# Kernel tuning notes

Measured on AMD Instinct MI355X. Metric: run time of the kernel, lower is better.

Reference implementation:

```python
import jax, jax.numpy as jnp
import numpy as np

R = 2
TAU = 0.1
EPS = 1e-7

# normalized 3x3 Sobel kernels (kornia SpatialGradient, normalized=True -> /8)
_GX = jnp.array([[-1., 0., 1.], [-2., 0., 2.], [-1., 0., 1.]], dtype=jnp.float32) / 8.0
_GY = _GX.T

K = 2 * R - 1  # 3
_HORIZ = jnp.zeros((K, K), jnp.float32).at[R - 1, :].set(1.0)
_VERT = jnp.zeros((K, K), jnp.float32).at[:, R - 1].set(1.0)
_LEAD = jnp.eye(K, dtype=jnp.float32)
_CNT = jnp.fliplr(jnp.eye(K, dtype=jnp.float32))


def _conv2d_same(x, k2d, mode):
    # depthwise 'same' cross-correlation, x: (B,C,H,W), k2d: (k,k)
    C = x.shape[1]
    p = k2d.shape[-1] // 2
    xp = jnp.pad(x, ((0, 0), (0, 0), (p, p), (p, p)), mode=mode)
    kern = jnp.broadcast_to(k2d[None, None], (C, 1) + k2d.shape)
    return jax.lax.conv_general_dilated(
        xp, kern, (1, 1), 'VALID',
        dimension_numbers=('NCHW', 'OIHW', 'NCHW'),
        feature_group_count=C)


def _grad_angles(t):
    # kornia SpatialGradient pads with replicate ('edge')
    gx = _conv2d_same(t, _GX, 'edge')
    gy = _conv2d_same(t, _GY, 'edge')
    grad_xx = _conv2d_same(gx, _GX, 'edge')
    grad_xy = _conv2d_same(gy, _GX, 'edge')
    grad_yy = _conv2d_same(gy, _GY, 'edge')
    theta = jnp.arctan(grad_yy * jnp.sign(-grad_xy + EPS) / (grad_xx + EPS))
    angle = theta * (180.0 / np.pi)
    return jnp.where(angle < 0, angle + 180.0, angle)


def _nms_loss(true_labels, pred_labels):
    angle = _grad_angles(true_labels)
    mask = (true_labels > 0).astype(jnp.float32)

    th_h = mask * (((angle >= 0) & (angle < 22.5)) | ((angle >= 157.5) & (angle < 180))).astype(jnp.float32)
    th_cd = mask * ((angle >= 22.5) & (angle < 67.5)).astype(jnp.float32)
    th_v = mask * ((angle >= 67.5) & (angle < 112.5)).astype(jnp.float32)
    th_ld = mask * ((angle > 112.5) & (angle < 157.5)).astype(jnp.float32)

    e = jnp.exp(pred_labels * TAU)

    def term(th, kern):
        f = _conv2d_same(e, kern, 'reflect')  # kornia filter2D default border 'reflect'
        return th * jnp.log(jnp.clip(e / (f + EPS), EPS, 1.0))

    total = (term(th_h, _HORIZ) + term(th_v, _VERT) +
             term(th_ld, _LEAD) + term(th_cd, _CNT))
    # sum over (C,H,W) per sample, mean over batch, negate
    return -jnp.mean(jnp.sum(total, axis=(1, 2, 3)))


def setup_inputs() -> dict:
    key = jax.random.key(0)
    k1, k2 = jax.random.split(key)
    B, C, H, W = 4, 19, 512, 512
    true_labels = jax.random.normal(k1, (B, C, H, W), dtype=jnp.float32)
    pred_labels = jax.random.normal(k2, (B, C, H, W), dtype=jnp.float32)
    return {"true_labels": true_labels, "pred_labels": pred_labels}


def reference(true_labels, pred_labels):
    return _nms_loss(true_labels, pred_labels)
```

## Files before the change

### kernel.cpp

```cpp
#include <hip/hip_runtime.h>

#define BAND 16
#define NITER (BAND + 4)
#define NSLOT 1024

__global__ __launch_bounds__(256) void nms_loss_kernel(
    const float* __restrict__ tl, const float* __restrict__ pl,
    double* __restrict__ acc_d, float* __restrict__ acc_f,
    int H, int W)
{
    const int y0  = blockIdx.x * BAND;
    const int ch  = blockIdx.y;
    const float* tc = tl + (size_t)ch * H * W;
    const float* pc = pl + (size_t)ch * H * W;
    const int tid  = threadIdx.x;
    const int lane = tid & 63;
    const int c0 = tid << 1;
    const int oa = min(max(c0 - 2, 0), W - 2);
    const int oc = min(c0 + 2, W - 2);
    const bool eL = (c0 == 0), eR = (c0 == W - 2);
    const float eL2 = eL ? 2.f : 0.f, eR2 = eR ? 2.f : 0.f;

    float P1h[5][2], P2h[5][2], P3h[5][2];
    float eh[3][4], tch[3][2];
    float t6[6], p6[6];

    #define LOADROW(I) {                                                            \
        int tr_ = y0 - 2 + (I); tr_ = min(max(tr_, 0), H - 1);                       \
        int pr_ = y0 - 3 + (I); pr_ = pr_ < 0 ? -pr_ : (pr_ >= H ? 2*H-2-pr_ : pr_); \
        const float* tb_ = tc + (size_t)tr_ * W;                                     \
        const float* pb_ = pc + (size_t)pr_ * W;                                     \
        float2 a_ = *(const float2*)(tb_ + oa), b_ = *(const float2*)(tb_ + c0),     \
               c_ = *(const float2*)(tb_ + oc);                                      \
        t6[0]=a_.x; t6[1]=a_.y; t6[2]=b_.x; t6[3]=b_.y; t6[4]=c_.x; t6[5]=c_.y;      \
        a_ = *(const float2*)(pb_ + oa); b_ = *(const float2*)(pb_ + c0);            \
        c_ = *(const float2*)(pb_ + oc);                                             \
        p6[0]=a_.x; p6[1]=a_.y; p6[2]=b_.x; p6[3]=b_.y; p6[4]=c_.x; p6[5]=c_.y;      \
        float g0_ = t6[0];                                                           \
        t6[0] = eL ? t6[1] : t6[0];                                                  \
        t6[1] = eL ? g0_   : t6[1];                                                  \
        float g4_ = t6[4];                                                           \
        t6[4] = eR ? t6[5] : t6[4];                                                  \
        t6[5] = eR ? g4_   : t6[5]; }

    #define CONSUME(K) {                                                             \
        eh[0][0]=eh[1][0]; eh[0][1]=eh[1][1]; eh[0][2]=eh[1][2]; eh[0][3]=eh[1][3];  \
        eh[1][0]=eh[2][0]; eh[1][1]=eh[2][1]; eh[1][2]=eh[2][2]; eh[1][3]=eh[2][3];  \
        tch[0][0]=tch[1][0]; tch[0][1]=tch[1][1];                                    \
        tch[1][0]=tch[2][0]; tch[1][1]=tch[2][1];                                    \
        float s04 = t6[0] + t6[4], s13 = t6[1] + t6[3];                              \
        P1h[K][0] = fmaf(-2.f, t6[2], s04);                                          \
        P3h[K][0] = fmaf(6.f, t6[2], fmaf(4.f, s13, s04));                           \
        P2h[K][0] = fmaf(2.f, t6[3] - t6[1], t6[4] - t6[0]);                         \
        float s04b = t6[1] + t6[5], s13b = t6[2] + t6[4];                            \
        P1h[K][1] = fmaf(-2.f, t6[3], s04b);                                         \
        P3h[K][1] = fmaf(6.f, t6[3], fmaf(4.f, s13b, s04b));                         \
        P2h[K][1] = fmaf(2.f, t6[4] - t6[2], t6[5] - t6[1]);                         \
        P1h[K][0] = fmaf(eL2, t6[2] - t6[3], P1h[K][0]);                             \
        P1h[K][1] = fmaf(eR2, t6[3] - t6[2], P1h[K][1]);                             \
        tch[2][0] = t6[2]; tch[2][1] = t6[3];                                        \
        eh[2][0] = __expf(0.1f * p6[1]);                                             \
        eh[2][1] = __expf(0.1f * p6[2]);                                             \
        eh[2][2] = __expf(0.1f * p6[3]);                                             \
        eh[2][3] = __expf(0.1f * p6[4]); }

    #define OUTPUT(I, K) if ((I) >= 4) {                                             \
        const int y = y0 + (I) - 4;                                                  \
        const int s0=((K)+1)%5, s1=((K)+2)%5, s2=((K)+3)%5, s3=((K)+4)%5, s4=(K);    \
        const bool ytop = (y == 0), ybot = (y == H - 1);                             \
        _Pragma("unroll")                                                            \
        for (int j = 0; j < 2; ++j) {                                                \
            float a04 = P1h[s0][j] + P1h[s4][j], a13 = P1h[s1][j] + P1h[s3][j];      \
            float xx = fmaf(6.f, P1h[s2][j], fmaf(4.f, a13, a04));                   \
            float xy = fmaf(2.f, P2h[s3][j] - P2h[s1][j], P2h[s4][j] - P2h[s0][j]);  \
            float yy = fmaf(-2.f, P3h[s2][j], P3h[s0][j] + P3h[s4][j]);              \
            if (ytop) {                                                              \
                xx += P1h[s3][j] - P1h[s2][j];                                       \
                xy += P2h[s3][j] - P2h[s2][j];                                       \
                yy += P3h[s2][j] - P3h[s3][j];                                       \
            } else if (ybot) {                                                       \
                xx += P1h[s1][j] - P1h[s2][j];                                       \
                xy += P2h[s2][j] - P2h[s1][j];                                       \
                yy += P3h[s2][j] - P3h[s1][j];                                       \
            }                                                                        \
            if (tch[0][j] > 0.f) {                                                   \
                float den = xx + 6.4e-6f;                                            \
                float sa  = 6.4e-6f - xy;                                            \
                float ax = fabsf(den), ay = fabsf(yy);                               \
                bool isH = ay < 0.41421356f * ax;                                    \
                bool isV = ay >= 2.41421356f * ax;                                   \
                bool qp  = ((yy * sa) * den) > 0.f;                                  \
                float ec = eh[1][j + 1];                                             \
                float n1 = isH ? eh[1][j + 2] : (isV ? eh[2][j + 1]                  \
                                : (qp ? eh[2][j] : eh[2][j + 2]));                   \
                float n2 = isH ? eh[1][j]     : (isV ? eh[0][j + 1]                  \
                                : (qp ? eh[0][j + 2] : eh[0][j]));                   \
                partial += __logf(__fdividef(ec, ec + n1 + n2 + 1e-7f));             \
            }                                                                        \
        } }

    LOADROW(0)

    float partial = 0.f;

    #pragma unroll 1
    for (int mm = 0; mm < 4; ++mm) {
        #pragma unroll
        for (int k = 0; k < 5; ++k) {
            const int i = mm * 5 + k;
            CONSUME(k)
            if (i + 1 < NITER) LOADROW(i + 1)
            OUTPUT(i, k)
        }
    }

    for (int off = 32; off > 0; off >>= 1)
        partial += __shfl_down(partial, off, 64);
    if (lane == 0) {
        int fid = (blockIdx.y * gridDim.x + blockIdx.x) * 4 + (tid >> 6);
        if (acc_d) atomicAdd(&acc_d[fid & (NSLOT - 1)], (double)partial);
        else       atomicAdd(acc_f, partial);
    }
}

__global__ void finalize_kernel(const double* acc_d, float* out,
                                int use_double, float inv_b)
{
    if (use_double) {
        int l = threadIdx.x;
        double s = 0.0;
        for (int i = l; i < NSLOT; i += 64) s += acc_d[i];
        for (int off = 32; off > 0; off >>= 1) s += __shfl_down(s, off, 64);
        if (l == 0) out[0] = (float)(-s * (double)inv_b);
    } else {
        if (threadIdx.x == 0) out[0] = -out[0] * inv_b;
    }
}

extern "C" void kernel_launch(void* const* d_in, const int* in_sizes, int n_in,
                              void* d_out, int out_size, void* d_ws, size_t ws_size,
                              hipStream_t stream)
{
    const float* tl = (const float*)d_in[0];
    const float* pl = (const float*)d_in[1];
    float* out = (float*)d_out;

    const int H = 512, W = 512, B = 4;

    double* acc_d = nullptr;
    float* acc_f = nullptr;
    int use_double = 0;
    if (ws_size >= NSLOT * sizeof(double)) {
        acc_d = (double*)d_ws;
        use_double = 1;
        hipMemsetAsync(acc_d, 0, NSLOT * sizeof(double), stream);
    } else {
        acc_f = out;
        hipMemsetAsync(out, 0, sizeof(float), stream);
    }

    dim3 grid(H / BAND, 76, 1);
    nms_loss_kernel<<<grid, 256, 0, stream>>>(tl, pl, acc_d, acc_f, H, W);
    finalize_kernel<<<1, 64, 0, stream>>>(acc_d, out, use_double, 1.0f / (float)B);
}
```

Measured before the change: 61.33 us.

## Use packed float2 math, fully unroll rows, and halve band height

Horizontal and vertical Sobel partial sums move to two-wide float vectors so the compiler can emit packed FP32 FMA/add instructions. The row loop is fully unrolled with modular register indexing, which removes the eh/tch shift copies. The band height drops from 16 to 8, doubling the number of blocks for more parallelism. The cost is more redundant halo row loads and exp work per output row, since each band rereads four extra rows.

After: 55.01 us, median of 2. 10.3% less time.

```diff
diff --git a/kernel.cpp b/kernel.cpp
--- a/kernel.cpp
+++ b/kernel.cpp
@@ -1,8 +1,15 @@
 #include <hip/hip_runtime.h>
 
-#define BAND 16
+#define BAND 8
 #define NITER (BAND + 4)
 #define NSLOT 1024
+
+typedef float v2f __attribute__((ext_vector_type(2)));
+
+__device__ __forceinline__ v2f fma2k(float k, v2f a, v2f b) {
+    v2f vk = {k, k};
+    return __builtin_elementwise_fma(vk, a, b);
+}
 
 __global__ __launch_bounds__(256) void nms_loss_kernel(
     const float* __restrict__ tl, const float* __restrict__ pl,
@@ -21,8 +28,9 @@
     const bool eL = (c0 == 0), eR = (c0 == W - 2);
     const float eL2 = eL ? 2.f : 0.f, eR2 = eR ? 2.f : 0.f;
 
-    float P1h[5][2], P2h[5][2], P3h[5][2];
-    float eh[3][4], tch[3][2];
+    v2f P1v[5], P2v[5], P3v[5];
+    float eh[3][4];
+    v2f tch[3];
     float t6[6], p6[6];
 
     #define LOADROW(I) {                                                            \
@@ -43,58 +51,57 @@
         t6[4] = eR ? t6[5] : t6[4];                                                  \
         t6[5] = eR ? g4_   : t6[5]; }
 
-    #define CONSUME(K) {                                                             \
-        eh[0][0]=eh[1][0]; eh[0][1]=eh[1][1]; eh[0][2]=eh[1][2]; eh[0][3]=eh[1][3];  \
-        eh[1][0]=eh[2][0]; eh[1][1]=eh[2][1]; eh[1][2]=eh[2][2]; eh[1][3]=eh[2][3];  \
-        tch[0][0]=tch[1][0]; tch[0][1]=tch[1][1];                                    \
-        tch[1][0]=tch[2][0]; tch[1][1]=tch[2][1];                                    \
-        float s04 = t6[0] + t6[4], s13 = t6[1] + t6[3];                              \
-        P1h[K][0] = fmaf(-2.f, t6[2], s04);                                          \
-        P3h[K][0] = fmaf(6.f, t6[2], fmaf(4.f, s13, s04));                           \
-        P2h[K][0] = fmaf(2.f, t6[3] - t6[1], t6[4] - t6[0]);                         \
-        float s04b = t6[1] + t6[5], s13b = t6[2] + t6[4];                            \
-        P1h[K][1] = fmaf(-2.f, t6[3], s04b);                                         \
-        P3h[K][1] = fmaf(6.f, t6[3], fmaf(4.f, s13b, s04b));                         \
-        P2h[K][1] = fmaf(2.f, t6[4] - t6[2], t6[5] - t6[1]);                         \
-        P1h[K][0] = fmaf(eL2, t6[2] - t6[3], P1h[K][0]);                             \
-        P1h[K][1] = fmaf(eR2, t6[3] - t6[2], P1h[K][1]);                             \
-        tch[2][0] = t6[2]; tch[2][1] = t6[3];                                        \
-        eh[2][0] = __expf(0.1f * p6[1]);                                             \
-        eh[2][1] = __expf(0.1f * p6[2]);                                             \
-        eh[2][2] = __expf(0.1f * p6[3]);                                             \
-        eh[2][3] = __expf(0.1f * p6[4]); }
+    #define CONSUME(SP, SE) {                                                        \
+        v2f Av = {t6[0], t6[1]}, Bv = {t6[1], t6[2]}, Cv = {t6[2], t6[3]};           \
+        v2f Dv = {t6[3], t6[4]}, Ev = {t6[4], t6[5]};                                \
+        v2f s04 = Av + Ev, s13 = Bv + Dv;                                            \
+        P1v[SP] = fma2k(-2.f, Cv, s04);                                     \
+        P3v[SP] = fma2k(6.f, Cv, fma2k(4.f, s13, s04));                     \
+        P2v[SP] = fma2k(2.f, Dv - Bv, Ev - Av);                             \
+        P1v[SP].x = fmaf(eL2, t6[2] - t6[3], P1v[SP].x);         \
+        P1v[SP].y = fmaf(eR2, t6[3] - t6[2], P1v[SP].y);                             \
+        tch[SE] = Cv;                                                                \
+        eh[SE][0] = __expf(0.1f * p6[1]);                                            \
+        eh[SE][1] = __expf(0.1f * p6[2]);                                            \
+        eh[SE][2] = __expf(0.1f * p6[3]);                                            \
+        eh[SE][3] = __expf(0.1f * p6[4]); }
 
-    #define OUTPUT(I, K) if ((I) >= 4) {                                             \
+    #define OUTPUT(I) if ((I) >= 4) {                                                \
         const int y = y0 + (I) - 4;                                                  \
-        const int s0=((K)+1)%5, s1=((K)+2)%5, s2=((K)+3)%5, s3=((K)+4)%5, s4=(K);    \
+        const int s0=((I)-4)%5, s1=((I)-3)%5, s2=((I)-2)%5, s3=((I)-1)%5, s4=(I)%5;  \
+        const int et=((I)-2)%3, em=((I)-1)%3, ebq=(I)%3;                             \
         const bool ytop = (y == 0), ybot = (y == H - 1);                             \
+        v2f a04 = P1v[s0] + P1v[s4], a13 = P1v[s1] + P1v[s3];                        \
+        v2f xx = fma2k(6.f, P1v[s2], fma2k(4.f, a13, a04));                          \
+        v2f xy = fma2k(2.f, P2v[s3] - P2v[s1], P2v[s4] - P2v[s0]);                   \
+        v2f yy = fma2k(-2.f, P3v[s2], P3v[s0] + P3v[s4]);                            \
+        if (ytop) {                                                                  \
+            xx += P1v[s3] - P1v[s2];                                                 \
+            xy += P2v[s3] - P2v[s2];                                                 \
+            yy += P3v[s2] - P3v[s3];                                                 \
+        } else if (ybot) {                                                           \
+            xx += P1v[s1] - P1v[s2];                                                 \
+            xy += P2v[s2] - P2v[s1];                                                 \
+            yy += P3v[s2] - P3v[s1];                                                 \
+        }                                                                            \
+        v2f den = xx + 6.4e-6f;                                                      \
+        v2f sa  = 6.4e-6f - xy;                                                      \
         _Pragma("unroll")                                                            \
         for (int j = 0; j < 2; ++j) {                                                \
-            float a04 = P1h[s0][j] + P1h[s4][j], a13 = P1h[s1][j] + P1h[s3][j];      \
-            float xx = fmaf(6.f, P1h[s2][j], fmaf(4.f, a13, a04));                   \
-            float xy = fmaf(2.f, P2h[s3][j] - P2h[s1][j], P2h[s4][j] - P2h[s0][j]);  \
-            float yy = fmaf(-2.f, P3h[s2][j], P3h[s0][j] + P3h[s4][j]);              \
-            if (ytop) {                                                              \
-                xx += P1h[s3][j] - P1h[s2][j];                                       \
-                xy += P2h[s3][j] - P2h[s2][j];                                       \
-                yy += P3h[s2][j] - P3h[s3][j];                                       \
-            } else if (ybot) {                                                       \
-                xx += P1h[s1][j] - P1h[s2][j];                                       \
-                xy += P2h[s2][j] - P2h[s1][j];                                       \
-                yy += P3h[s2][j] - P3h[s1][j];                                       \
-            }                                                                        \
-            if (tch[0][j] > 0.f) {                                                   \
-                float den = xx + 6.4e-6f;                                            \
-                float sa  = 6.4e-6f - xy;                                            \
-                float ax = fabsf(den), ay = fabsf(yy);                               \
+            float tcv = j ? tch[et].y : tch[et].x;                                   \
+            if (tcv > 0.f) {                                                         \
+                float dj = j ? den.y : den.x;                                        \
+                float sj = j ? sa.y  : sa.x;                                         \
+                float yj = j ? yy.y  : yy.x;                                         \
+                float ax = fabsf(dj), ay = fabsf(yj);                                \
                 bool isH = ay < 0.41421356f * ax;                                    \
                 bool isV = ay >= 2.41421356f * ax;                                   \
-                bool qp  = ((yy * sa) * den) > 0.f;                                  \
-                float ec = eh[1][j + 1];                                             \
-                float n1 = isH ? eh[1][j + 2] : (isV ? eh[2][j + 1]                  \
-                                : (qp ? eh[2][j] : eh[2][j + 2]));                   \
-                float n2 = isH ? eh[1][j]     : (isV ? eh[0][j + 1]                  \
-                                : (qp ? eh[0][j + 2] : eh[0][j]));                   \
+                bool qp  = ((yj * sj) * dj) > 0.f;                                   \
+                float ec = eh[em][j + 1];                                            \
+                float n1 = isH ? eh[em][j + 2] : (isV ? eh[ebq][j + 1]               \
+                                : (qp ? eh[ebq][j] : eh[ebq][j + 2]));               \
+                float n2 = isH ? eh[em][j]     : (isV ? eh[et][j + 1]                \
+                                : (qp ? eh[et][j + 2] : eh[et][j]));                 \
                 partial += __logf(__fdividef(ec, ec + n1 + n2 + 1e-7f));             \
             }                                                                        \
         } }
@@ -103,15 +110,11 @@
 
     float partial = 0.f;
 
-    #pragma unroll 1
-    for (int mm = 0; mm < 4; ++mm) {
-        #pragma unroll
-        for (int k = 0; k < 5; ++k) {
-            const int i = mm * 5 + k;
-            CONSUME(k)
-            if (i + 1 < NITER) LOADROW(i + 1)
-            OUTPUT(i, k)
-        }
+    #pragma unroll
+    for (int i = 0; i < NITER; ++i) {
+        CONSUME(i % 5, i % 3)
+        if (i + 1 < NITER) LOADROW(i + 1)
+        OUTPUT(i)
     }
 
     for (int off = 32; off > 0; off >>= 1)
```
